# Optimization experiments

Hardware: AMD Instinct MI355X
Metric: run time of the kernel (lower is better)

Reference implementation:

```python
import jax, jax.numpy as jnp
import numpy as np

H = 4      # SSM / attn heads (d_model/headdim = 256/64)
WIN = 4    # attention window over bands


def _ln(x, g, b):
    m = jnp.mean(x, -1, keepdims=True)
    v = jnp.mean((x - m) ** 2, -1, keepdims=True)
    return (x - m) * jax.lax.rsqrt(v + 1e-5) * g + b


def setup_inputs() -> dict:
    key = jax.random.key(0)
    ks = jax.random.split(key, 24)
    def rn(i, shape, s=0.05):
        return jax.random.normal(ks[i], shape, jnp.float32) * s
    B, T, K, D = 2, 256, 8, 256
    return {
        "z": rn(0, (B, T, K, D), 1.0),
        "ln1_g": jnp.ones((D,), jnp.float32), "ln1_b": jnp.zeros((D,), jnp.float32),
        "Wx": rn(1, (D, D)), "conv_w": rn(2, (D, 4), 0.3), "Wz": rn(3, (D, D)),
        "Wb": rn(4, (D, H * 128)), "Wc": rn(5, (D, H * 128)), "Wdt": rn(6, (D, H)),
        "dt_bias": rn(7, (H,), 0.5), "A_log": rn(8, (H,), 0.5), "theta": rn(9, (H,), 1.0),
        "D_skip": rn(10, (H,), 1.0), "mimo_U": rn(11, (H, H), 0.5), "mimo_V": rn(12, (H, H), 0.5),
        "Wout": rn(13, (D, D)),
        "ln2_g": jnp.ones((D,), jnp.float32), "ln2_b": jnp.zeros((D,), jnp.float32),
        "attn_in_w": rn(14, (3 * D, D)), "attn_in_b": rn(15, (3 * D,), 0.02),
        "attn_out_w": rn(16, (D, D)), "attn_out_b": jnp.zeros((D,), jnp.float32),
        "ln3_g": jnp.ones((D,), jnp.float32), "ln3_b": jnp.zeros((D,), jnp.float32),
        "Wg": rn(17, (D, 4 * D)), "Wu": rn(18, (D, 4 * D)), "Wd": rn(19, (4 * D, D)),
    }


def _forward(z, ln1_g, ln1_b, Wx, conv_w, Wz, Wb, Wc, Wdt, dt_bias, A_log, theta,
             D_skip, mimo_U, mimo_V, Wout, ln2_g, ln2_b, attn_in_w, attn_in_b,
             attn_out_w, attn_out_b, ln3_g, ln3_b, Wg, Wu, Wd):
    B, T, K, D = z.shape
    P = D // H
    N = Wb.shape[1] // H
    # ---------- (a) intra-band Mamba3 (complex MIMO selective scan) ----------
    u = _ln(z, ln1_g, ln1_b)
    u = jnp.transpose(u, (0, 2, 1, 3)).reshape(B * K, T, D)   # [BK,T,D]
    x = u @ Wx
    # causal depthwise conv1d, kernel 4
    xp = jnp.pad(x, ((0, 0), (3, 0), (0, 0)))
    x = sum(xp[:, k:k + T, :] * conv_w[:, k] for k in range(4))
    x = jax.nn.silu(x)
    xh = x.reshape(B * K, T, H, P)
    Bm = (u @ Wb).reshape(B * K, T, H, N)
    Cm = (u @ Wc).reshape(B * K, T, H, N)
    Mmix = mimo_U @ mimo_V.T                                  # rank-r cross-head coupling
    Bm = jnp.einsum('hg,btgn->bthn', Mmix, Bm)
    dt = jax.nn.softplus(u @ Wdt + dt_bias)                   # [BK,T,H]
    A = -jnp.exp(A_log)                                       # stable real decay
    mag = jnp.exp(dt * A)
    ph = dt * theta                                           # harmonic rotation
    ar, ai = mag * jnp.cos(ph), mag * jnp.sin(ph)
    xs = tuple(jnp.moveaxis(t, 1, 0) for t in (xh, Bm, Cm, dt, ar, ai))
    h0 = jnp.zeros((B * K, H, N, P), x.dtype)

    def step(carry, s):
        h_re, h_im = carry
        xt, bt, ct, dtt, art, ait = s
        dBx = (dtt[:, :, None, None] * bt[:, :, :, None]) * xt[:, :, None, :]
        nr = art[:, :, None, None] * h_re - ait[:, :, None, None] * h_im + dBx
        ni = art[:, :, None, None] * h_im + ait[:, :, None, None] * h_re
        return (nr, ni), jnp.einsum('bhn,bhnp->bhp', ct, nr)   # Re(C . h)

    _, ys = jax.lax.scan(step, (h0, h0), xs)                  # ys: [T,BK,H,P]
    y = jnp.moveaxis(ys, 0, 1) + D_skip[None, None, :, None] * xh
    y = y.reshape(B * K, T, D) * jax.nn.silu(u @ Wz)
    y = y @ Wout
    z = z + jnp.transpose(y.reshape(B, K, T, D), (0, 2, 1, 3))
    # ---------- (b) inter-band windowed attention ----------
    zn = _ln(z, ln2_g, ln2_b).reshape(B * T, K, D)
    qkv = zn @ attn_in_w.T + attn_in_b
    q, k_, v = jnp.split(qkv, 3, axis=-1)
    hd = D // H
    def hs(t):
        return t.reshape(B * T, K // WIN, WIN, H, hd).transpose(0, 1, 3, 2, 4)
    q, k_, v = hs(q), hs(k_), hs(v)
    s = jnp.einsum('mwhqd,mwhkd->mwhqk', q, k_) * jnp.float32(1.0 / np.sqrt(hd))
    a = jax.nn.softmax(s, axis=-1)
    o = jnp.einsum('mwhqk,mwhkd->mwhqd', a, v).transpose(0, 1, 3, 2, 4).reshape(B * T, K, D)
    z = z + (o @ attn_out_w.T + attn_out_b).reshape(B, T, K, D)
    # ---------- (c) SwiGLU FFN ----------
    zf = _ln(z, ln3_g, ln3_b)
    z = z + (jax.nn.silu(zf @ Wg) * (zf @ Wu)) @ Wd
    return z


def reference(z, ln1_g, ln1_b, Wx, conv_w, Wz, Wb, Wc, Wdt, dt_bias, A_log, theta,
              D_skip, mimo_U, mimo_V, Wout, ln2_g, ln2_b, attn_in_w, attn_in_b,
              attn_out_w, attn_out_b, ln3_g, ln3_b, Wg, Wu, Wd):
    return _forward(z, ln1_g, ln1_b, Wx, conv_w, Wz, Wb, Wc, Wdt, dt_bias, A_log,
                    theta, D_skip, mimo_U, mimo_V, Wout, ln2_g, ln2_b, attn_in_w,
                    attn_in_b, attn_out_w, attn_out_b, ln3_g, ln3_b, Wg, Wu, Wd)
```

## Files before the change

### kernel.cpp

```cpp
#include <hip/hip_runtime.h>
#include <hip/hip_bf16.h>
#include <math.h>

typedef __hip_bfloat16 bf16;
typedef __attribute__((ext_vector_type(8))) short s16x8;
typedef __attribute__((ext_vector_type(4))) float f32x4;

__device__ __forceinline__ float siluf(float x) { return x / (1.f + __expf(-x)); }
__device__ __forceinline__ float bits2f(unsigned short u) {
    union { float f; unsigned i; } v; v.i = ((unsigned)u) << 16; return v.f;
}
__device__ __forceinline__ unsigned short f2bits(float f) {
    return (unsigned short)__bfloat16_as_ushort(__float2bfloat16(f));
}

#define KFL 1024
#define OFF_UB   (768*KFL)
#define OFF_DTV  (1280*KFL)
#define OFF_BMB  (1344*KFL)
#define OFF_CMB  (2368*KFL)
#define OFF_ZGB  (3392*KFL)
#define OFF_XB   (3904*KFL)
#define OFF_X2T  (4928*KFL)
#define OFF_P    (5440*KFL)
#define OFF_YGB  (7488*KFL)
#define OFF_Z2   (8000*KFL)
#define OFF_ZFB  (9024*KFL)
#define OFF_GG   OFF_BMB

#define W_BCZX 0
#define W_OUT  393216
#define W_QKV  458752
#define W_AO   655360
#define W_GU   720896
#define W_D    1245184

__global__ __launch_bounds__(256) void prep_ln1_kernel(
    const float* __restrict__ Wx, const float* __restrict__ Wb,
    const float* __restrict__ Wc, const float* __restrict__ Wz,
    const float* __restrict__ Wo, const float* __restrict__ Wqkv,
    const float* __restrict__ Wao, const float* __restrict__ Wg,
    const float* __restrict__ Wu, const float* __restrict__ Wd,
    const float* __restrict__ U, const float* __restrict__ V,
    unsigned short* __restrict__ wout,
    const float* __restrict__ z, const float* __restrict__ g1,
    const float* __restrict__ b1, const float* __restrict__ Wdt,
    const float* __restrict__ dt_bias,
    unsigned short* __restrict__ u, float4* __restrict__ dtv4)
{
    __shared__ __align__(16) float smem[64 * 65];
    int blk = blockIdx.x;
    int tid = threadIdx.x;
    if (blk < 368) {
        if (blk >= 304) {
            int off = blk - 304;
            const float* src; int dst, base;
            if (off < 48) { src = Wqkv; dst = W_QKV; base = off * 4096; }
            else          { src = Wao;  dst = W_AO;  base = (off - 48) * 4096; }
            #pragma unroll
            for (int i = 0; i < 16; i++) {
                int idx = base + tid + i * 256;
                wout[dst + idx] = f2bits(src[idx]);
            }
            return;
        }
        float* lds = smem;
        const float* src; int srcN, n0, sc0, k0, dstoff, dstK, mix = 0, t;
        if (blk < 32)       { t = blk;       src = Wb; srcN = 512;  dstoff = W_BCZX; dstK = 256;
                              n0 = (t >> 2) * 64;        sc0 = 0; k0 = (t & 3) * 64; mix = 1; }
        else if (blk < 64)  { t = blk - 32;  src = Wc; srcN = 512;  dstoff = W_BCZX; dstK = 256;
                              n0 = 512 + (t >> 2) * 64;  sc0 = (t >> 2) * 64; k0 = (t & 3) * 64; }
        else if (blk < 80)  { t = blk - 64;  src = Wz; srcN = 256;  dstoff = W_BCZX; dstK = 256;
                              n0 = 1024 + (t >> 2) * 64; sc0 = (t >> 2) * 64; k0 = (t & 3) * 64; }
        else if (blk < 96)  { t = blk - 80;  src = Wx; srcN = 256;  dstoff = W_BCZX; dstK = 256;
                              n0 = 1280 + (t >> 2) * 64; sc0 = (t >> 2) * 64; k0 = (t & 3) * 64; }
        else if (blk < 112) { t = blk - 96;  src = Wo; srcN = 256;  dstoff = W_OUT;  dstK = 256;
                              n0 = (t >> 2) * 64;        sc0 = n0; k0 = (t & 3) * 64; }
        else if (blk < 176) { t = blk - 112; src = Wg; srcN = 1024; dstoff = W_GU;   dstK = 256;
                              n0 = (t >> 2) * 64;        sc0 = n0; k0 = (t & 3) * 64; }
        else if (blk < 240) { t = blk - 176; src = Wu; srcN = 1024; dstoff = W_GU;   dstK = 256;
                              n0 = 1024 + (t >> 2) * 64; sc0 = (t >> 2) * 64; k0 = (t & 3) * 64; }
        else                { t = blk - 240; src = Wd; srcN = 256;  dstoff = W_D;    dstK = 1024;
                              n0 = (t >> 4) * 64;        sc0 = n0; k0 = (t & 15) * 64; }
        if (mix) {
            int h = n0 >> 7, scol = n0 & 127;
            float mm[4];
            #pragma unroll
            for (int g = 0; g < 4; g++) {
                float s = 0.f;
                #pragma unroll
                for (int j = 0; j < 4; j++) s += U[h * 4 + j] * V[g * 4 + j];
                mm[g] = s;
            }
            #pragma unroll
            for (int i = 0; i < 16; i++) {
                int idx = tid + i * 256;
                int kk = idx >> 6, nn = idx & 63;
                const float* row = src + (size_t)(k0 + kk) * 512 + scol + nn;
                lds[kk * 65 + nn] = mm[0] * row[0] + mm[1] * row[128]
                                  + mm[2] * row[256] + mm[3] * row[384];
            }
        } else {
            #pragma unroll
            for (int i = 0; i < 16; i++) {
                int idx = tid + i * 256;
                int kk = idx >> 6, nn = idx & 63;
                lds[kk * 65 + nn] = src[(size_t)(k0 + kk) * srcN + sc0 + nn];
            }
        }
        __syncthreads();
        #pragma unroll
        for (int i = 0; i < 16; i++) {
            int idx = tid + i * 256;
            int nn = idx >> 6, kk = idx & 63;
            wout[dstoff + (size_t)(n0 + nn) * dstK + k0 + kk] = f2bits(lds[kk * 65 + nn]);
        }
        return;
    }
    int r = blk - 368;
    float* lds = smem;
    float* dts = smem + 4;
    int t = r & 255, bk = r >> 8;
    int b_ = bk >> 3, k = bk & 7;
    int srcr = ((b_ * 256 + t) * 8 + k) * 256;
    int d = tid;
    float x = z[srcr + d];
    float v = x;
    #pragma unroll
    for (int off = 32; off; off >>= 1) v += __shfl_xor(v, off, 64);
    if ((d & 63) == 0) lds[d >> 6] = v;
    __syncthreads();
    float mean = (lds[0] + lds[1] + lds[2] + lds[3]) * (1.f / 256.f);
    __syncthreads();
    float c = x - mean;
    v = c * c;
    #pragma unroll
    for (int off = 32; off; off >>= 1) v += __shfl_xor(v, off, 64);
    if ((d & 63) == 0) lds[d >> 6] = v;
    __syncthreads();
    float var = (lds[0] + lds[1] + lds[2] + lds[3]) * (1.f / 256.f);
    float uval = c * rsqrtf(var + 1e-5f) * g1[d] + b1[d];
    u[r * 256 + d] = f2bits(uval);
    float4 wv = *(const float4*)(Wdt + d * 4);
    float q0 = uval * wv.x, q1 = uval * wv.y, q2 = uval * wv.z, q3 = uval * wv.w;
    #pragma unroll
    for (int off = 32; off; off >>= 1) {
        q0 += __shfl_xor(q0, off, 64);
        q1 += __shfl_xor(q1, off, 64);
        q2 += __shfl_xor(q2, off, 64);
        q3 += __shfl_xor(q3, off, 64);
    }
    if ((d & 63) == 0) {
        int w = d >> 6;
        dts[w * 4 + 0] = q0; dts[w * 4 + 1] = q1;
        dts[w * 4 + 2] = q2; dts[w * 4 + 3] = q3;
    }
    __syncthreads();
    if (d == 0) {
        float dv[4];
        #pragma unroll
        for (int h = 0; h < 4; h++) {
            float xx = dts[h] + dts[4 + h] + dts[8 + h] + dts[12 + h] + dt_bias[h];
            dv[h] = (xx > 20.f) ? xx : log1pf(__expf(xx));
        }
        dtv4[r] = make_float4(dv[0], dv[1], dv[2], dv[3]);
    }
}

__global__ __launch_bounds__(256) void gemm_bczx(
    const unsigned short* __restrict__ A, const unsigned short* __restrict__ Bt,
    unsigned short* __restrict__ bmb, unsigned short* __restrict__ cmb,
    unsigned short* __restrict__ zgb, unsigned short* __restrict__ xb)
{
    __shared__ __align__(16) unsigned short As[64 * 72];
    __shared__ __align__(16) unsigned short Bs[128 * 72];
    const int K = 256;
    int tid = threadIdx.x;
    int n0 = blockIdx.x * 128, m0 = blockIdx.y * 64;
    int w = tid >> 6, l = tid & 63;
    int mwave = (w >> 1) * 32, nwave = (w & 1) * 64;
    f32x4 acc[2][4] = {};
    int srow = tid >> 3, sc = (tid & 7) * 8;
    const unsigned short* Ap = A + (size_t)(m0 + srow) * K + sc;
    const unsigned short* Bp = Bt + (size_t)(n0 + srow) * K + sc;
    int lq = l & 15, lh = l >> 4;
    uint4 a0 = *(const uint4*)(Ap);
    uint4 a1 = *(const uint4*)(Ap + (size_t)32 * K);
    uint4 b0 = *(const uint4*)(Bp);
    uint4 b1 = *(const uint4*)(Bp + (size_t)32 * K);
    uint4 b2 = *(const uint4*)(Bp + (size_t)64 * K);
    uint4 b3 = *(const uint4*)(Bp + (size_t)96 * K);
    for (int k0 = 0; k0 < K; k0 += 64) {
        if (k0) __syncthreads();
        *(uint4*)&As[srow * 72 + sc] = a0;
        *(uint4*)&As[(srow + 32) * 72 + sc] = a1;
        *(uint4*)&Bs[srow * 72 + sc] = b0;
        *(uint4*)&Bs[(srow + 32) * 72 + sc] = b1;
        *(uint4*)&Bs[(srow + 64) * 72 + sc] = b2;
        *(uint4*)&Bs[(srow + 96) * 72 + sc] = b3;
        __syncthreads();
        if (k0 + 64 < K) {
            a0 = *(const uint4*)(Ap + k0 + 64);
            a1 = *(const uint4*)(Ap + (size_t)32 * K + k0 + 64);
            b0 = *(const uint4*)(Bp + k0 + 64);
            b1 = *(const uint4*)(Bp + (size_t)32 * K + k0 + 64);
            b2 = *(const uint4*)(Bp + (size_t)64 * K + k0 + 64);
            b3 = *(const uint4*)(Bp + (size_t)96 * K + k0 + 64);
        }
        #pragma unroll
        for (int kk = 0; kk < 2; kk++) {
            int kof = kk * 32 + lh * 8;
            s16x8 bfr[4];
            #pragma unroll
            for (int nf = 0; nf < 4; nf++)
                bfr[nf] = *(const s16x8*)&Bs[(nwave + nf * 16 + lq) * 72 + kof];
            #pragma unroll
            for (int mf = 0; mf < 2; mf++) {
                s16x8 af = *(const s16x8*)&As[(mwave + mf * 16 + lq) * 72 + kof];
                #pragma unroll
                for (int nf = 0; nf < 4; nf++)
                    acc[mf][nf] = __builtin_amdgcn_mfma_f32_16x16x32_bf16(af, bfr[nf], acc[mf][nf], 0, 0, 0);
            }
        }
    }
    #pragma unroll
    for (int mf = 0; mf < 2; mf++) {
        #pragma unroll
        for (int nf = 0; nf < 4; nf++) {
            int n = n0 + nwave + nf * 16 + lq;
            #pragma unroll
            for (int r = 0; r < 4; r++) {
                int m = m0 + mwave + mf * 16 + lh * 4 + r;
                float v = acc[mf][nf][r];
                if (n < 512)       bmb[(size_t)m * 512 + n] = f2bits(v);
                else if (n < 1024) cmb[(size_t)m * 512 + (n - 512)] = f2bits(v);
                else if (n < 1280) zgb[(size_t)m * 256 + (n - 1024)] = f2bits(siluf(v));
                else               xb[(size_t)m * 256 + (n - 1280)] = f2bits(v);
            }
        }
    }
}

__global__ __launch_bounds__(256) void s_conv_kernel(
    const unsigned short* __restrict__ cmb, const unsigned short* __restrict__ bmb,
    const float4* __restrict__ dtv4, const float* __restrict__ A_log,
    const float* __restrict__ theta, unsigned short* __restrict__ P,
    const unsigned short* __restrict__ xb, const float* __restrict__ cw,
    unsigned short* __restrict__ x2t)
{
    __shared__ __align__(16) char smem[39936];
    int blk = blockIdx.x;
    int tid = threadIdx.x;
    if (blk >= 192) {
        int c = blk - 192;
        int bhid = c >> 2, tt = c & 3;
        int bk = bhid >> 2, h = bhid & 3;
        int t0 = tt * 64;
        float* tile = (float*)smem;
        #pragma unroll
        for (int i = 0; i < 17; i++) {
            int idx = tid + i * 256;
            if (idx < 67 * 64) {
                int tr = idx >> 6, dd = idx & 63;
                int t = t0 - 3 + tr;
                tile[tr * 65 + dd] = (t >= 0)
                    ? bits2f(xb[(size_t)(bk * 256 + t) * 256 + h * 64 + dd]) : 0.f;
            }
        }
        __syncthreads();
        int wv_ = tid >> 6, lt = tid & 63;
        #pragma unroll 4
        for (int pi = 0; pi < 16; pi++) {
            int p = wv_ * 16 + pi;
            float4 wv = *(const float4*)(cw + (h * 64 + p) * 4);
            float acc = tile[lt * 65 + p] * wv.x + tile[(lt + 1) * 65 + p] * wv.y +
                        tile[(lt + 2) * 65 + p] * wv.z + tile[(lt + 3) * 65 + p] * wv.w;
            x2t[(size_t)(bhid * 64 + p) * 256 + t0 + lt] = f2bits(siluf(acc));
        }
        return;
    }
    int map = blk >> 6;
    int bh = blk & 63;
    int bx = (map == 2) ? 1 : 0;
    int by = (map == 0) ? 0 : 1;
    int bk = bh >> 2, h = bh & 3;
    unsigned short* As = (unsigned short*)smem;
    unsigned short* Bs = As + 128 * 72;
    float* mAs = (float*)(smem + 36864);
    float* phs = mAs + 256;
    float* dss = phs + 256;
    int srow = tid >> 3, sc = (tid & 7) * 8;
    const unsigned short* Ap = cmb + (size_t)(bk * 256 + by * 128 + srow) * 512 + h * 128 + sc;
    const unsigned short* Bp = bmb + (size_t)(bk * 256 + bx * 128 + srow) * 512 + h * 128 + sc;
    uint4 a0 = *(const uint4*)(Ap);
    uint4 a1 = *(const uint4*)(Ap + (size_t)32 * 512);
    uint4 a2 = *(const uint4*)(Ap + (size_t)64 * 512);
    uint4 a3 = *(const uint4*)(Ap + (size_t)96 * 512);
    uint4 b0 = *(const uint4*)(Bp);
    uint4 b1 = *(const uint4*)(Bp + (size_t)32 * 512);
    uint4 b2 = *(const uint4*)(Bp + (size_t)64 * 512);
    uint4 b3 = *(const uint4*)(Bp + (size_t)96 * 512);
    {
        float4 dv = dtv4[bk * 256 + tid];
        float dth = (h == 0) ? dv.x : (h == 1) ? dv.y : (h == 2) ? dv.z : dv.w;
        float Ah = -__expf(A_log[h]);
        float th = theta[h];
        float a = dth * Ah, p = dth * th;
        dss[tid] = dth;
        int lane = tid & 63, wv = tid >> 6;
        #pragma unroll
        for (int off = 1; off < 64; off <<= 1) {
            float ta = __shfl_up(a, off, 64);
            float tp = __shfl_up(p, off, 64);
            if (lane >= off) { a += ta; p += tp; }
        }
        if (lane == 63) { mAs[wv] = a; phs[wv] = p; }
        __syncthreads();
        float offA = 0.f, offP = 0.f;
        #pragma unroll
        for (int j = 0; j < 3; j++)
            if (j < wv) { offA += mAs[j]; offP += phs[j]; }
        __syncthreads();
        mAs[tid] = a + offA;
        phs[tid] = p + offP;
        __syncthreads();
    }
    int w = tid >> 6, l = tid & 63;
    int mwave = (w >> 1) * 64, nwave = (w & 1) * 64;
    int lq = l & 15, lh = l >> 4;
    unsigned short* Pout = P + (size_t)bh * 65536;
    f32x4 acc[4][4] = {};
    for (int k0 = 0; k0 < 128; k0 += 64) {
        __syncthreads();
        *(uint4*)&As[srow * 72 + sc] = a0;
        *(uint4*)&As[(srow + 32) * 72 + sc] = a1;
        *(uint4*)&As[(srow + 64) * 72 + sc] = a2;
        *(uint4*)&As[(srow + 96) * 72 + sc] = a3;
        *(uint4*)&Bs[srow * 72 + sc] = b0;
        *(uint4*)&Bs[(srow + 32) * 72 + sc] = b1;
        *(uint4*)&Bs[(srow + 64) * 72 + sc] = b2;
        *(uint4*)&Bs[(srow + 96) * 72 + sc] = b3;
        __syncthreads();
        if (k0 + 64 < 128) {
            a0 = *(const uint4*)(Ap + k0 + 64);
            a1 = *(const uint4*)(Ap + (size_t)32 * 512 + k0 + 64);
            a2 = *(const uint4*)(Ap + (size_t)64 * 512 + k0 + 64);
            a3 = *(const uint4*)(Ap + (size_t)96 * 512 + k0 + 64);
            b0 = *(const uint4*)(Bp + k0 + 64);
            b1 = *(const uint4*)(Bp + (size_t)32 * 512 + k0 + 64);
            b2 = *(const uint4*)(Bp + (size_t)64 * 512 + k0 + 64);
            b3 = *(const uint4*)(Bp + (size_t)96 * 512 + k0 + 64);
        }
        #pragma unroll
        for (int kk = 0; kk < 2; kk++) {
            int kof = kk * 32 + lh * 8;
            s16x8 bfr[4];
            #pragma unroll
            for (int nf = 0; nf < 4; nf++)
                bfr[nf] = *(const s16x8*)&Bs[(nwave + nf * 16 + lq) * 72 + kof];
            #pragma unroll
            for (int mf = 0; mf < 4; mf++) {
                s16x8 af = *(const s16x8*)&As[(mwave + mf * 16 + lq) * 72 + kof];
                #pragma unroll
                for (int nf = 0; nf < 4; nf++)
                    acc[mf][nf] = __builtin_amdgcn_mfma_f32_16x16x32_bf16(af, bfr[nf], acc[mf][nf], 0, 0, 0);
            }
        }
    }
    #pragma unroll
    for (int mf = 0; mf < 4; mf++) {
        float tmv[4], tpv[4]; int tg[4];
        #pragma unroll
        for (int r = 0; r < 4; r++) {
            tg[r] = by * 128 + mwave + mf * 16 + lh * 4 + r;
            tmv[r] = mAs[tg[r]];
            tpv[r] = phs[tg[r]];
        }
        #pragma unroll
        for (int nf = 0; nf < 4; nf++) {
            int s = bx * 128 + nwave + nf * 16 + lq;
            float ms = mAs[s];
            float ps = phs[s];
            float ds = dss[s];
            #pragma unroll
            for (int r = 0; r < 4; r++) {
                float wgt = (s <= tg[r])
                    ? __expf(tmv[r] - ms) * __cosf(tpv[r] - ps) * ds : 0.f;
                Pout[tg[r] * 256 + s] = f2bits(acc[mf][nf][r] * wgt);
            }
        }
    }
}

__global__ __launch_bounds__(256) void gemm_y(
    const unsigned short* __restrict__ P, const unsigned short* __restrict__ x2t,
    const unsigned short* __restrict__ zgb, const float* __restrict__ Dsk,
    unsigned short* __restrict__ ygb)
{
    int by = blockIdx.x, bh = blockIdx.y;
    int bk = bh >> 2, h = bh & 3;
    int t0 = by * 32;
    int tid = threadIdx.x;
    int w = tid >> 6, l = tid & 63;
    int mw = (w >> 1) * 16, nw = (w & 1) * 32;
    int lq = l & 15, lh = l >> 4;
    __shared__ __align__(16) unsigned short As[32 * 72];
    __shared__ __align__(16) unsigned short Bs[64 * 72];
    f32x4 acc[2] = {};
    int srow = tid >> 3, sc = (tid & 7) * 8;
    const unsigned short* Ap = P + (size_t)bh * 65536 + (size_t)(t0 + srow) * 256 + sc;
    const unsigned short* Bp = x2t + (size_t)bh * 16384 + (size_t)srow * 256 + sc;
    int kmax = ((by >> 1) + 1) * 64;
    uint4 a0 = *(const uint4*)(Ap);
    uint4 b0 = *(const uint4*)(Bp);
    uint4 b1 = *(const uint4*)(Bp + (size_t)32 * 256);
    for (int k0 = 0; k0 < kmax; k0 += 64) {
        if (k0) __syncthreads();
        *(uint4*)&As[(srow & 31) * 72 + sc] = a0;
        *(uint4*)&Bs[srow * 72 + sc] = b0;
        *(uint4*)&Bs[(srow + 32) * 72 + sc] = b1;
        __syncthreads();
        if (k0 + 64 < kmax) {
            a0 = *(const uint4*)(Ap + k0 + 64);
            b0 = *(const uint4*)(Bp + k0 + 64);
            b1 = *(const uint4*)(Bp + (size_t)32 * 256 + k0 + 64);
        }
        #pragma unroll
        for (int kk = 0; kk < 2; kk++) {
            int kof = kk * 32 + lh * 8;
            s16x8 af = *(const s16x8*)&As[(mw + lq) * 72 + kof];
            #pragma unroll
            for (int nf = 0; nf < 2; nf++) {
                s16x8 bf = *(const s16x8*)&Bs[(nw + nf * 16 + lq) * 72 + kof];
                acc[nf] = __builtin_amdgcn_mfma_f32_16x16x32_bf16(af, bf, acc[nf], 0, 0, 0);
            }
        }
    }
    float dsk = Dsk[h];
    #pragma unroll
    for (int nf = 0; nf < 2; nf++) {
        int p = nw + nf * 16 + lq;
        #pragma unroll
        for (int r = 0; r < 4; r++) {
            int t = t0 + mw + lh * 4 + r;
            float xv = bits2f(x2t[(size_t)bh * 16384 + p * 256 + t]);
            float zg = bits2f(zgb[(size_t)(bk * 256 + t) * 256 + h * 64 + p]);
            ygb[(size_t)(bk * 256 + t) * 256 + h * 64 + p] =
                f2bits((acc[nf][r] + dsk * xv) * zg);
        }
    }
}

__global__ __launch_bounds__(512) void mid_kernel(
    const unsigned short* __restrict__ ygb, const unsigned short* __restrict__ wts,
    const float* __restrict__ zin,
    const float* __restrict__ g2, const float* __restrict__ b2,
    const float* __restrict__ qbias, const float* __restrict__ obias,
    const float* __restrict__ g3, const float* __restrict__ b3,
    float* __restrict__ z2, unsigned short* __restrict__ zfb)
{
    __shared__ __align__(16) char smem[65024];
    unsigned short* Bs = (unsigned short*)smem;
    unsigned short* As = (unsigned short*)(smem + 36864);
    unsigned short* zn = (unsigned short*)(smem + 39168);
    float* z1s = (float*)(smem + 47616);
    float (*partS)[8] = (float(*)[8])(smem + 64000);
    float (*partQ)[8] = (float(*)[8])(smem + 64512);
    unsigned short* qk = (unsigned short*)smem;

    const int K = 256;
    int tid = threadIdx.x;
    int m0 = blockIdx.x * 16;
    int w = tid >> 6, l = tid & 63;
    int nw = w * 32;
    int lq = l & 15, lh = l >> 4;
    int srow = tid >> 3, sc = (tid & 7) * 8;

    const unsigned short* BpO  = wts + W_OUT + (size_t)srow * K + sc;
    const unsigned short* BpQ0 = wts + W_QKV + (size_t)srow * K + sc;
    const unsigned short* BpQ1 = BpQ0 + (size_t)256 * K;
    const unsigned short* BpQ2 = BpQ0 + (size_t)512 * K;
    const unsigned short* BpA  = wts + W_AO + (size_t)srow * K + sc;

    uint4 wA0, wA1, wA2, wA3, wB0, wB1, wB2, wB3;

#define LOADW(P, BASE, KO) do { \
    P##0 = *(const uint4*)((BASE) + (KO)); \
    P##1 = *(const uint4*)((BASE) + (size_t)64 * K + (KO)); \
    P##2 = *(const uint4*)((BASE) + (size_t)128 * K + (KO)); \
    P##3 = *(const uint4*)((BASE) + (size_t)192 * K + (KO)); \
} while (0)
#define STORE_BS(P) do { \
    *(uint4*)&Bs[srow * 72 + sc] = P##0; \
    *(uint4*)&Bs[(srow + 64) * 72 + sc] = P##1; \
    *(uint4*)&Bs[(srow + 128) * 72 + sc] = P##2; \
    *(uint4*)&Bs[(srow + 192) * 72 + sc] = P##3; \
} while (0)
#define MM_ZN(AQ, KO) do { \
    _Pragma("unroll") \
    for (int kk = 0; kk < 2; kk++) { \
        int kof = kk * 32 + lh * 8; \
        s16x8 af = *(const s16x8*)&zn[lq * 264 + (KO) + kof]; \
        _Pragma("unroll") \
        for (int nf = 0; nf < 2; nf++) { \
            s16x8 bf = *(const s16x8*)&Bs[(nw + nf * 16 + lq) * 72 + kof]; \
            AQ[nf] = __builtin_amdgcn_mfma_f32_16x16x32_bf16(af, bf, AQ[nf], 0, 0, 0); \
        } \
    } \
} while (0)
#define MM_AS(AQ) do { \
    _Pragma("unroll") \
    for (int kk = 0; kk < 2; kk++) { \
        int kof = kk * 32 + lh * 8; \
        s16x8 af = *(const s16x8*)&As[lq * 72 + kof]; \
        _Pragma("unroll") \
        for (int nf = 0; nf < 2; nf++) { \
            s16x8 bf = *(const s16x8*)&Bs[(nw + nf * 16 + lq) * 72 + kof]; \
            AQ[nf] = __builtin_amdgcn_mfma_f32_16x16x32_bf16(af, bf, AQ[nf], 0, 0, 0); \
        } \
    } \
} while (0)

    f32x4 acc1[2] = {};
    {
        int rb = m0 + (srow & 15);
        int irow = ((rb >> 11) * 8 + (rb & 7)) * 256 + ((rb >> 3) & 255);
        const unsigned short* Ap = ygb + (size_t)irow * K + sc;
        LOADW(wA, BpO, 0);
        LOADW(wB, BpO, 64);
        uint4 aP = *(const uint4*)(Ap);
        uint4 aQ;
        __syncthreads();
        if (tid < 128) *(uint4*)&As[srow * 72 + sc] = aP;
        STORE_BS(wA);
        __syncthreads();
        aQ = *(const uint4*)(Ap + 64);
        LOADW(wA, BpO, 128);
        MM_AS(acc1);
        __syncthreads();
        if (tid < 128) *(uint4*)&As[srow * 72 + sc] = aQ;
        STORE_BS(wB);
        __syncthreads();
        aP = *(const uint4*)(Ap + 128);
        LOADW(wB, BpO, 192);
        MM_AS(acc1);
        __syncthreads();
        if (tid < 128) *(uint4*)&As[srow * 72 + sc] = aP;
        STORE_BS(wA);
        __syncthreads();
        aQ = *(const uint4*)(Ap + 192);
        LOADW(wA, BpQ0, 0);
        MM_AS(acc1);
        __syncthreads();
        if (tid < 128) *(uint4*)&As[srow * 72 + sc] = aQ;
        STORE_BS(wB);
        __syncthreads();
        LOADW(wB, BpQ0, 64);
        MM_AS(acc1);
        #pragma unroll
        for (int r = 0; r < 4; r++) {
            int row = lh * 4 + r;
            float s = 0.f, q = 0.f;
            #pragma unroll
            for (int nf = 0; nf < 2; nf++) {
                float v = acc1[nf][r] + zin[(size_t)(m0 + row) * 256 + nw + nf * 16 + lq];
                acc1[nf][r] = v;
                s += v; q += v * v;
            }
            #pragma unroll
            for (int off = 1; off < 16; off <<= 1) {
                s += __shfl_xor(s, off, 64);
                q += __shfl_xor(q, off, 64);
            }
            if (lq == 0) { partS[row][w] = s; partQ[row][w] = q; }
        }
        __syncthreads();
        float gv[2], bbv[2];
        #pragma unroll
        for (int nf = 0; nf < 2; nf++) {
            gv[nf] = g2[nw + nf * 16 + lq];
            bbv[nf] = b2[nw + nf * 16 + lq];
        }
        #pragma unroll
        for (int r = 0; r < 4; r++) {
            int row = lh * 4 + r;
            float sum = 0.f, sq = 0.f;
            #pragma unroll
            for (int j = 0; j < 8; j++) { sum += partS[row][j]; sq += partQ[row][j]; }
            float mean = sum * (1.f / 256.f);
            float var = sq * (1.f / 256.f) - mean * mean;
            float rstd = rsqrtf(var + 1e-5f);
            #pragma unroll
            for (int nf = 0; nf < 2; nf++) {
                int n = nw + nf * 16 + lq;
                float v = acc1[nf][r];
                z1s[row * 256 + n] = v;
                zn[row * 264 + n] = f2bits((v - mean) * rstd * gv[nf] + bbv[nf]);
            }
        }
    }

    f32x4 aq0[2] = {}, aq1[2] = {}, aq2[2] = {};
#define RND(P, AQ, KO, NBASE, NKO) do { \
    __syncthreads(); \
    STORE_BS(P); \
    __syncthreads(); \
    LOADW(P, NBASE, NKO); \
    MM_ZN(AQ, KO); \
} while (0)
#define RND_NL(P, AQ, KO) do { \
    __syncthreads(); \
    STORE_BS(P); \
    __syncthreads(); \
    MM_ZN(AQ, KO); \
} while (0)
    RND(wA, aq0, 0,   BpQ0, 128);
    RND(wB, aq0, 64,  BpQ0, 192);
    RND(wA, aq0, 128, BpQ1, 0);
    RND(wB, aq0, 192, BpQ1, 64);
    RND(wA, aq1, 0,   BpQ1, 128);
    RND(wB, aq1, 64,  BpQ1, 192);
    RND(wA, aq1, 128, BpQ2, 0);
    RND(wB, aq1, 192, BpQ2, 64);
    RND(wA, aq2, 0,   BpQ2, 128);
    RND(wB, aq2, 64,  BpQ2, 192);
    RND(wA, aq2, 128, BpA, 0);
    RND(wB, aq2, 192, BpA, 64);

    __syncthreads();
#define QKV_STORE(PIDX, AQ) do { \
    _Pragma("unroll") \
    for (int nf = 0; nf < 2; nf++) { \
        int n = (PIDX) * 256 + nw + nf * 16 + lq; \
        float bb = qbias[n]; \
        _Pragma("unroll") \
        for (int r = 0; r < 4; r++) \
            qk[(lh * 4 + r) * 776 + n] = f2bits(AQ[nf][r] + bb); \
    } \
} while (0)
    QKV_STORE(0, aq0);
    QKV_STORE(1, aq1);
    QKV_STORE(2, aq2);
#undef QKV_STORE
    __syncthreads();
    {
        int hh = w & 3;
        int half = w >> 2;
        int d = l;
        #pragma unroll
        for (int wi = 0; wi < 2; wi++) {
            int w4 = half * 2 + wi;
            int r0 = w4 * 4;
            float qv[4], kv[4], vv[4];
            #pragma unroll
            for (int j = 0; j < 4; j++) {
                qv[j] = bits2f(qk[(r0 + j) * 776 + hh * 64 + d]);
                kv[j] = bits2f(qk[(r0 + j) * 776 + 256 + hh * 64 + d]);
                vv[j] = bits2f(qk[(r0 + j) * 776 + 512 + hh * 64 + d]);
            }
            float sc_[4][4];
            #pragma unroll
            for (int qi = 0; qi < 4; qi++)
                #pragma unroll
                for (int ki = 0; ki < 4; ki++) {
                    float v = qv[qi] * kv[ki];
                    #pragma unroll
                    for (int off = 32; off; off >>= 1) v += __shfl_xor(v, off, 64);
                    sc_[qi][ki] = v * 0.125f;
                }
            #pragma unroll
            for (int qi = 0; qi < 4; qi++) {
                float mx = fmaxf(fmaxf(sc_[qi][0], sc_[qi][1]), fmaxf(sc_[qi][2], sc_[qi][3]));
                float e0 = __expf(sc_[qi][0] - mx), e1 = __expf(sc_[qi][1] - mx);
                float e2 = __expf(sc_[qi][2] - mx), e3 = __expf(sc_[qi][3] - mx);
                float inv = 1.f / (e0 + e1 + e2 + e3);
                float ov = (e0 * vv[0] + e1 * vv[1] + e2 * vv[2] + e3 * vv[3]) * inv;
                zn[(r0 + qi) * 264 + hh * 64 + d] = f2bits(ov);
            }
        }
    }

    {
        f32x4 ac4[2] = {};
        RND(wA, ac4, 0,  BpA, 128);
        RND(wB, ac4, 64, BpA, 192);
        RND_NL(wA, ac4, 128);
        RND_NL(wB, ac4, 192);
        float bv[2], gv[2], bbv[2];
        #pragma unroll
        for (int nf = 0; nf < 2; nf++) {
            int n = nw + nf * 16 + lq;
            bv[nf] = obias[n];
            gv[nf] = g3[n];
            bbv[nf] = b3[n];
        }
        #pragma unroll
        for (int r = 0; r < 4; r++) {
            int row = lh * 4 + r;
            float s = 0.f, q = 0.f;
            #pragma unroll
            for (int nf = 0; nf < 2; nf++) {
                float v = ac4[nf][r] + bv[nf] + z1s[row * 256 + nw + nf * 16 + lq];
                ac4[nf][r] = v;
                s += v; q += v * v;
            }
            #pragma unroll
            for (int off = 1; off < 16; off <<= 1) {
                s += __shfl_xor(s, off, 64);
                q += __shfl_xor(q, off, 64);
            }
            if (lq == 0) { partS[row][w] = s; partQ[row][w] = q; }
        }
        __syncthreads();
        #pragma unroll
        for (int r = 0; r < 4; r++) {
            int row = lh * 4 + r;
            float sum = 0.f, sq = 0.f;
            #pragma unroll
            for (int j = 0; j < 8; j++) { sum += partS[row][j]; sq += partQ[row][j]; }
            float mean = sum * (1.f / 256.f);
            float var = sq * (1.f / 256.f) - mean * mean;
            float rstd = rsqrtf(var + 1e-5f);
            size_t ro = (size_t)(m0 + row) * 256;
            #pragma unroll
            for (int nf = 0; nf < 2; nf++) {
                int n = nw + nf * 16 + lq;
                float v = ac4[nf][r];
                z2[ro + n] = v;
                zfb[ro + n] = f2bits((v - mean) * rstd * gv[nf] + bbv[nf]);
            }
        }
    }
#undef RND
#undef RND_NL
#undef LOADW
#undef STORE_BS
#undef MM_ZN
#undef MM_AS
}

__global__ __launch_bounds__(256) void gemm_gu2(
    const unsigned short* __restrict__ A, const unsigned short* __restrict__ Wgu,
    unsigned short* __restrict__ gg)
{
    const int K = 256;
    __shared__ __align__(16) unsigned short As[64 * 72];
    __shared__ __align__(16) unsigned short Bgs[64 * 72];
    __shared__ __align__(16) unsigned short Bus[64 * 72];
    int tid = threadIdx.x;
    int n0 = blockIdx.x * 64, m0 = blockIdx.y * 64;
    int w = tid >> 6, l = tid & 63;
    int mwave = (w >> 1) * 32, nwave = (w & 1) * 32;
    int lq = l & 15, lh = l >> 4;
    f32x4 ag[2][2] = {}, au[2][2] = {};
    int srow = tid >> 3, sc = (tid & 7) * 8;
    const unsigned short* Ap = A + (size_t)(m0 + srow) * K + sc;
    const unsigned short* Bgp = Wgu + (size_t)(n0 + srow) * K + sc;
    const unsigned short* Bup = Wgu + (size_t)(1024 + n0 + srow) * K + sc;
    uint4 a0 = *(const uint4*)(Ap);
    uint4 a1 = *(const uint4*)(Ap + (size_t)32 * K);
    uint4 bg0 = *(const uint4*)(Bgp);
    uint4 bg1 = *(const uint4*)(Bgp + (size_t)32 * K);
    uint4 bu0 = *(const uint4*)(Bup);
    uint4 bu1 = *(const uint4*)(Bup + (size_t)32 * K);
    for (int k0 = 0; k0 < K; k0 += 64) {
        if (k0) __syncthreads();
        *(uint4*)&As[srow * 72 + sc] = a0;
        *(uint4*)&As[(srow + 32) * 72 + sc] = a1;
        *(uint4*)&Bgs[srow * 72 + sc] = bg0;
        *(uint4*)&Bgs[(srow + 32) * 72 + sc] = bg1;
        *(uint4*)&Bus[srow * 72 + sc] = bu0;
        *(uint4*)&Bus[(srow + 32) * 72 + sc] = bu1;
        __syncthreads();
        if (k0 + 64 < K) {
            a0 = *(const uint4*)(Ap + k0 + 64);
            a1 = *(const uint4*)(Ap + (size_t)32 * K + k0 + 64);
            bg0 = *(const uint4*)(Bgp + k0 + 64);
            bg1 = *(const uint4*)(Bgp + (size_t)32 * K + k0 + 64);
            bu0 = *(const uint4*)(Bup + k0 + 64);
            bu1 = *(const uint4*)(Bup + (size_t)32 * K + k0 + 64);
        }
        #pragma unroll
        for (int kk = 0; kk < 2; kk++) {
            int kof = kk * 32 + lh * 8;
            s16x8 bgr[2], bur[2];
            #pragma unroll
            for (int nf = 0; nf < 2; nf++) {
                bgr[nf] = *(const s16x8*)&Bgs[(nwave + nf * 16 + lq) * 72 + kof];
                bur[nf] = *(const s16x8*)&Bus[(nwave + nf * 16 + lq) * 72 + kof];
            }
            #pragma unroll
            for (int mf = 0; mf < 2; mf++) {
                s16x8 af = *(const s16x8*)&As[(mwave + mf * 16 + lq) * 72 + kof];
                #pragma unroll
                for (int nf = 0; nf < 2; nf++) {
                    ag[mf][nf] = __builtin_amdgcn_mfma_f32_16x16x32_bf16(af, bgr[nf], ag[mf][nf], 0, 0, 0);
                    au[mf][nf] = __builtin_amdgcn_mfma_f32_16x16x32_bf16(af, bur[nf], au[mf][nf], 0, 0, 0);
                }
            }
        }
    }
    #pragma unroll
    for (int mf = 0; mf < 2; mf++) {
        #pragma unroll
        for (int nf = 0; nf < 2; nf++) {
            int n = n0 + nwave + nf * 16 + lq;
            #pragma unroll
            for (int r = 0; r < 4; r++) {
                int m = m0 + mwave + mf * 16 + lh * 4 + r;
                gg[(size_t)m * 1024 + n] = f2bits(siluf(ag[mf][nf][r]) * au[mf][nf][r]);
            }
        }
    }
}

__global__ __launch_bounds__(256) void gemm_d2(
    const unsigned short* __restrict__ gg, const unsigned short* __restrict__ Bt,
    const float* __restrict__ resid, float* __restrict__ out)
{
    __shared__ __align__(16) unsigned short As[64 * 72];
    __shared__ __align__(16) unsigned short Bs[32 * 72];
    const int K = 1024, N = 256;
    int tid = threadIdx.x;
    int n0 = blockIdx.x * 32, m0 = blockIdx.y * 64;
    int w = tid >> 6, l = tid & 63;
    int mw = (w >> 1) * 32, nw = (w & 1) * 16;
    f32x4 acc[2] = {};
    int srow = tid >> 3, sc = (tid & 7) * 8;
    const unsigned short* Ap = gg + (size_t)(m0 + srow) * K + sc;
    const unsigned short* Bp = Bt + (size_t)(n0 + (srow & 31)) * K + sc;
    int lq = l & 15, lh = l >> 4;
    uint4 xA0 = *(const uint4*)(Ap);
    uint4 xA1 = *(const uint4*)(Ap + (size_t)32 * K);
    uint4 yA  = *(const uint4*)(Bp);
    uint4 xB0 = *(const uint4*)(Ap + 64);
    uint4 xB1 = *(const uint4*)(Ap + (size_t)32 * K + 64);
    uint4 yB  = *(const uint4*)(Bp + 64);
    for (int k0 = 0; k0 < K; k0 += 128) {
        __syncthreads();
        *(uint4*)&As[srow * 72 + sc] = xA0;
        *(uint4*)&As[(srow + 32) * 72 + sc] = xA1;
        *(uint4*)&Bs[(srow & 31) * 72 + sc] = yA;
        __syncthreads();
        if (k0 + 128 < K) {
            xA0 = *(const uint4*)(Ap + k0 + 128);
            xA1 = *(const uint4*)(Ap + (size_t)32 * K + k0 + 128);
            yA  = *(const uint4*)(Bp + k0 + 128);
        }
        #pragma unroll
        for (int kk = 0; kk < 2; kk++) {
            int kof = kk * 32 + lh * 8;
            s16x8 bf = *(const s16x8*)&Bs[(nw + lq) * 72 + kof];
            #pragma unroll
            for (int mf = 0; mf < 2; mf++) {
                s16x8 af = *(const s16x8*)&As[(mw + mf * 16 + lq) * 72 + kof];
                acc[mf] = __builtin_amdgcn_mfma_f32_16x16x32_bf16(af, bf, acc[mf], 0, 0, 0);
            }
        }
        __syncthreads();
        *(uint4*)&As[srow * 72 + sc] = xB0;
        *(uint4*)&As[(srow + 32) * 72 + sc] = xB1;
        *(uint4*)&Bs[(srow & 31) * 72 + sc] = yB;
        __syncthreads();
        if (k0 + 192 < K) {
            xB0 = *(const uint4*)(Ap + k0 + 192);
            xB1 = *(const uint4*)(Ap + (size_t)32 * K + k0 + 192);
            yB  = *(const uint4*)(Bp + k0 + 192);
        }
        #pragma unroll
        for (int kk = 0; kk < 2; kk++) {
            int kof = kk * 32 + lh * 8;
            s16x8 bf = *(const s16x8*)&Bs[(nw + lq) * 72 + kof];
            #pragma unroll
            for (int mf = 0; mf < 2; mf++) {
                s16x8 af = *(const s16x8*)&As[(mw + mf * 16 + lq) * 72 + kof];
                acc[mf] = __builtin_amdgcn_mfma_f32_16x16x32_bf16(af, bf, acc[mf], 0, 0, 0);
            }
        }
    }
    int n = n0 + nw + lq;
    #pragma unroll
    for (int mf = 0; mf < 2; mf++) {
        #pragma unroll
        for (int r = 0; r < 4; r++) {
            int m = m0 + mw + mf * 16 + lh * 4 + r;
            out[(size_t)m * N + n] = acc[mf][r] + resid[(size_t)m * N + n];
        }
    }
}

extern "C" void kernel_launch(void* const* d_in, const int* in_sizes, int n_in,
                              void* d_out, int out_size, void* d_ws, size_t ws_size,
                              hipStream_t stream)
{
    const float* z         = (const float*)d_in[0];
    const float* ln1_g     = (const float*)d_in[1];
    const float* ln1_b     = (const float*)d_in[2];
    const float* Wx        = (const float*)d_in[3];
    const float* conv_w    = (const float*)d_in[4];
    const float* Wz        = (const float*)d_in[5];
    const float* Wb        = (const float*)d_in[6];
    const float* Wc        = (const float*)d_in[7];
    const float* Wdt       = (const float*)d_in[8];
    const float* dt_bias   = (const float*)d_in[9];
    const float* A_log     = (const float*)d_in[10];
    const float* theta     = (const float*)d_in[11];
    const float* D_skip    = (const float*)d_in[12];
    const float* mimo_U    = (const float*)d_in[13];
    const float* mimo_V    = (const float*)d_in[14];
    const float* Wout      = (const float*)d_in[15];
    const float* ln2_g     = (const float*)d_in[16];
    const float* ln2_b     = (const float*)d_in[17];
    const float* attn_in_w = (const float*)d_in[18];
    const float* attn_in_b = (const float*)d_in[19];
    const float* attn_out_w= (const float*)d_in[20];
    const float* attn_out_b= (const float*)d_in[21];
    const float* ln3_g     = (const float*)d_in[22];
    const float* ln3_b     = (const float*)d_in[23];
    const float* Wg        = (const float*)d_in[24];
    const float* Wu        = (const float*)d_in[25];
    const float* Wd        = (const float*)d_in[26];

    float* W = (float*)d_ws;
    unsigned short* wts = (unsigned short*)W;
    unsigned short* ub  = (unsigned short*)(W + OFF_UB);
    float4* dtv4        = (float4*)(W + OFF_DTV);
    unsigned short* bmb = (unsigned short*)(W + OFF_BMB);
    unsigned short* cmb = (unsigned short*)(W + OFF_CMB);
    unsigned short* zgb = (unsigned short*)(W + OFF_ZGB);
    unsigned short* xb  = (unsigned short*)(W + OFF_XB);
    unsigned short* x2t = (unsigned short*)(W + OFF_X2T);
    unsigned short* pbuf= (unsigned short*)(W + OFF_P);
    unsigned short* ygb = (unsigned short*)(W + OFF_YGB);
    float* z2           = W + OFF_Z2;
    unsigned short* zfb = (unsigned short*)(W + OFF_ZFB);
    unsigned short* gg  = (unsigned short*)(W + OFF_GG);

    prep_ln1_kernel<<<4464, 256, 0, stream>>>(
        Wx, Wb, Wc, Wz, Wout, attn_in_w, attn_out_w, Wg, Wu, Wd, mimo_U, mimo_V,
        wts, z, ln1_g, ln1_b, Wdt, dt_bias, ub, dtv4);
    gemm_bczx<<<dim3(12, 64), 256, 0, stream>>>(ub, wts + W_BCZX, bmb, cmb, zgb, xb);
    s_conv_kernel<<<448, 256, 0, stream>>>(cmb, bmb, dtv4, A_log, theta, pbuf,
                                           xb, conv_w, x2t);
    gemm_y<<<dim3(8, 64), 256, 0, stream>>>(pbuf, x2t, zgb, D_skip, ygb);
    mid_kernel<<<256, 512, 0, stream>>>(ygb, wts, z, ln2_g, ln2_b,
                                        attn_in_b, attn_out_b, ln3_g, ln3_b,
                                        z2, zfb);
    gemm_gu2<<<dim3(16, 64), 256, 0, stream>>>(zfb, wts + W_GU, gg);
    gemm_d2<<<dim3(8, 64), 256, 0, stream>>>(gg, wts + W_D, z2, (float*)d_out);
}
```

Measured before the change: 190.5 us.

## Fuse SSM score, conv and Y GEMM into one kernel keeping P in LDS

Merges the score/conv kernel and the gemm_y kernel into a single score_kernel. Each block computes a 64-row band of the causal decay-weighted C·B^T matrix into shared memory, recomputes the depthwise conv plus SiLU of x per chunk, then multiplies P by the conv output and applies the D-skip and gate. This removes the global P and x2t round trips and one kernel launch. The cost is redundant conv recomputation across blocks, only 256 blocks, and uneven causal work per block.

```diff
diff --git a/kernel.cpp b/kernel.cpp
--- a/kernel.cpp
+++ b/kernel.cpp
@@ -21,8 +21,6 @@
 #define OFF_CMB  (2368*KFL)
 #define OFF_ZGB  (3392*KFL)
 #define OFF_XB   (3904*KFL)
-#define OFF_X2T  (4928*KFL)
-#define OFF_P    (5440*KFL)
 #define OFF_YGB  (7488*KFL)
 #define OFF_Z2   (8000*KFL)
 #define OFF_ZFB  (9024*KFL)
@@ -241,144 +239,107 @@
     }
 }
 
-__global__ __launch_bounds__(256) void s_conv_kernel(
+__global__ __launch_bounds__(512) void score_kernel(
     const unsigned short* __restrict__ cmb, const unsigned short* __restrict__ bmb,
     const float4* __restrict__ dtv4, const float* __restrict__ A_log,
-    const float* __restrict__ theta, unsigned short* __restrict__ P,
+    const float* __restrict__ theta,
     const unsigned short* __restrict__ xb, const float* __restrict__ cw,
-    unsigned short* __restrict__ x2t)
+    const unsigned short* __restrict__ zgb, const float* __restrict__ Dsk,
+    unsigned short* __restrict__ ygb)
 {
-    __shared__ __align__(16) char smem[39936];
-    int blk = blockIdx.x;
-    int tid = threadIdx.x;
-    if (blk >= 192) {
-        int c = blk - 192;
-        int bhid = c >> 2, tt = c & 3;
-        int bk = bhid >> 2, h = bhid & 3;
-        int t0 = tt * 64;
-        float* tile = (float*)smem;
-        #pragma unroll
-        for (int i = 0; i < 17; i++) {
-            int idx = tid + i * 256;
-            if (idx < 67 * 64) {
-                int tr = idx >> 6, dd = idx & 63;
-                int t = t0 - 3 + tr;
-                tile[tr * 65 + dd] = (t >= 0)
-                    ? bits2f(xb[(size_t)(bk * 256 + t) * 256 + h * 64 + dd]) : 0.f;
-            }
-        }
-        __syncthreads();
-        int wv_ = tid >> 6, lt = tid & 63;
-        #pragma unroll 4
-        for (int pi = 0; pi < 16; pi++) {
-            int p = wv_ * 16 + pi;
-            float4 wv = *(const float4*)(cw + (h * 64 + p) * 4);
-            float acc = tile[lt * 65 + p] * wv.x + tile[(lt + 1) * 65 + p] * wv.y +
-                        tile[(lt + 2) * 65 + p] * wv.z + tile[(lt + 3) * 65 + p] * wv.w;
-            x2t[(size_t)(bhid * 64 + p) * 256 + t0 + lt] = f2bits(siluf(acc));
-        }
-        return;
-    }
-    int map = blk >> 6;
-    int bh = blk & 63;
-    int bx = (map == 2) ? 1 : 0;
-    int by = (map == 0) ? 0 : 1;
-    int bk = bh >> 2, h = bh & 3;
-    unsigned short* As = (unsigned short*)smem;
-    unsigned short* Bs = As + 128 * 72;
-    float* mAs = (float*)(smem + 36864);
+    __shared__ __align__(16) char smem[62976];
+    unsigned short* Pl  = (unsigned short*)smem;
+    unsigned short* As2 = (unsigned short*)(smem + 33792);
+    unsigned short* Bs  = (unsigned short*)(smem + 50688);
+    unsigned short* Xc  = (unsigned short*)(smem + 33792);
+    float* mAs = (float*)(smem + 59904);
     float* phs = mAs + 256;
     float* dss = phs + 256;
-    int srow = tid >> 3, sc = (tid & 7) * 8;
-    const unsigned short* Ap = cmb + (size_t)(bk * 256 + by * 128 + srow) * 512 + h * 128 + sc;
-    const unsigned short* Bp = bmb + (size_t)(bk * 256 + bx * 128 + srow) * 512 + h * 128 + sc;
-    uint4 a0 = *(const uint4*)(Ap);
-    uint4 a1 = *(const uint4*)(Ap + (size_t)32 * 512);
-    uint4 a2 = *(const uint4*)(Ap + (size_t)64 * 512);
-    uint4 a3 = *(const uint4*)(Ap + (size_t)96 * 512);
-    uint4 b0 = *(const uint4*)(Bp);
-    uint4 b1 = *(const uint4*)(Bp + (size_t)32 * 512);
-    uint4 b2 = *(const uint4*)(Bp + (size_t)64 * 512);
-    uint4 b3 = *(const uint4*)(Bp + (size_t)96 * 512);
+
+    int by = blockIdx.x;
+    int bh = blockIdx.y;
+    int bk = bh >> 2, h = bh & 3;
+    int tid = threadIdx.x;
+    int w = tid >> 6, l = tid & 63;
+    int lq = l & 15, lh = l >> 4;
+    int srow2 = tid >> 3, sc2 = (tid & 7) * 8;
+
+    uint4 ax0, ax1;
     {
-        float4 dv = dtv4[bk * 256 + tid];
-        float dth = (h == 0) ? dv.x : (h == 1) ? dv.y : (h == 2) ? dv.z : dv.w;
+        int uid0 = tid, uid1 = tid + 512;
+        ax0 = *(const uint4*)(cmb + (size_t)(bk * 256 + by * 64 + (uid0 >> 4)) * 512 + h * 128 + (uid0 & 15) * 8);
+        ax1 = *(const uint4*)(cmb + (size_t)(bk * 256 + by * 64 + (uid1 >> 4)) * 512 + h * 128 + (uid1 & 15) * 8);
+    }
+    uint4 bl = *(const uint4*)(bmb + (size_t)(bk * 256 + srow2) * 512 + h * 128 + sc2);
+    float4 cwv = *(const float4*)(cw + (h * 64 + l) * 4);
+
+    {
+        float dth = 0.f;
+        if (tid < 256) {
+            float4 dv = dtv4[bk * 256 + tid];
+            dth = (h == 0) ? dv.x : (h == 1) ? dv.y : (h == 2) ? dv.z : dv.w;
+            dss[tid] = dth;
+        }
         float Ah = -__expf(A_log[h]);
         float th = theta[h];
-        float a = dth * Ah, p = dth * th;
-        dss[tid] = dth;
+        float sa = dth * Ah, sp = dth * th;
         int lane = tid & 63, wv = tid >> 6;
         #pragma unroll
         for (int off = 1; off < 64; off <<= 1) {
-            float ta = __shfl_up(a, off, 64);
-            float tp = __shfl_up(p, off, 64);
-            if (lane >= off) { a += ta; p += tp; }
-        }
-        if (lane == 63) { mAs[wv] = a; phs[wv] = p; }
+            float ta = __shfl_up(sa, off, 64);
+            float tp = __shfl_up(sp, off, 64);
+            if (lane >= off) { sa += ta; sp += tp; }
+        }
+        if (tid < 256 && lane == 63) { mAs[wv] = sa; phs[wv] = sp; }
         __syncthreads();
         float offA = 0.f, offP = 0.f;
         #pragma unroll
         for (int j = 0; j < 3; j++)
             if (j < wv) { offA += mAs[j]; offP += phs[j]; }
         __syncthreads();
-        mAs[tid] = a + offA;
-        phs[tid] = p + offP;
-        __syncthreads();
-    }
-    int w = tid >> 6, l = tid & 63;
-    int mwave = (w >> 1) * 64, nwave = (w & 1) * 64;
-    int lq = l & 15, lh = l >> 4;
-    unsigned short* Pout = P + (size_t)bh * 65536;
-    f32x4 acc[4][4] = {};
-    for (int k0 = 0; k0 < 128; k0 += 64) {
-        __syncthreads();
-        *(uint4*)&As[srow * 72 + sc] = a0;
-        *(uint4*)&As[(srow + 32) * 72 + sc] = a1;
-        *(uint4*)&As[(srow + 64) * 72 + sc] = a2;
-        *(uint4*)&As[(srow + 96) * 72 + sc] = a3;
-        *(uint4*)&Bs[srow * 72 + sc] = b0;
-        *(uint4*)&Bs[(srow + 32) * 72 + sc] = b1;
-        *(uint4*)&Bs[(srow + 64) * 72 + sc] = b2;
-        *(uint4*)&Bs[(srow + 96) * 72 + sc] = b3;
-        __syncthreads();
-        if (k0 + 64 < 128) {
-            a0 = *(const uint4*)(Ap + k0 + 64);
-            a1 = *(const uint4*)(Ap + (size_t)32 * 512 + k0 + 64);
-            a2 = *(const uint4*)(Ap + (size_t)64 * 512 + k0 + 64);
-            a3 = *(const uint4*)(Ap + (size_t)96 * 512 + k0 + 64);
-            b0 = *(const uint4*)(Bp + k0 + 64);
-            b1 = *(const uint4*)(Bp + (size_t)32 * 512 + k0 + 64);
-            b2 = *(const uint4*)(Bp + (size_t)64 * 512 + k0 + 64);
-            b3 = *(const uint4*)(Bp + (size_t)96 * 512 + k0 + 64);
-        }
-        #pragma unroll
-        for (int kk = 0; kk < 2; kk++) {
-            int kof = kk * 32 + lh * 8;
-            s16x8 bfr[4];
-            #pragma unroll
-            for (int nf = 0; nf < 4; nf++)
-                bfr[nf] = *(const s16x8*)&Bs[(nwave + nf * 16 + lq) * 72 + kof];
-            #pragma unroll
-            for (int mf = 0; mf < 4; mf++) {
-                s16x8 af = *(const s16x8*)&As[(mwave + mf * 16 + lq) * 72 + kof];
+        if (tid < 256) { mAs[tid] = sa + offA; phs[tid] = sp + offP; }
+    }
+    {
+        int uid0 = tid, uid1 = tid + 512;
+        *(uint4*)&As2[(uid0 >> 4) * 132 + (uid0 & 15) * 8] = ax0;
+        *(uint4*)&As2[(uid1 >> 4) * 132 + (uid1 & 15) * 8] = ax1;
+    }
+
+    int mwP = (w & 3) * 16, nwP = (w >> 2) * 32;
+    for (int nc = 0; nc <= by; nc++) {
+        f32x4 pacc[2] = {};
+        #pragma unroll
+        for (int k0 = 0; k0 < 128; k0 += 64) {
+            __syncthreads();
+            *(uint4*)&Bs[srow2 * 72 + sc2] = bl;
+            __syncthreads();
+            {
+                int nnc = nc, nk0 = k0 + 64;
+                if (nk0 == 128) { nnc = nc + 1; nk0 = 0; }
+                if (nnc <= by)
+                    bl = *(const uint4*)(bmb + (size_t)(bk * 256 + nnc * 64 + srow2) * 512 + h * 128 + nk0 + sc2);
+            }
+            #pragma unroll
+            for (int kk = 0; kk < 2; kk++) {
+                int kof = kk * 32 + lh * 8;
+                s16x8 af = *(const s16x8*)&As2[(mwP + lq) * 132 + k0 + kof];
                 #pragma unroll
-                for (int nf = 0; nf < 4; nf++)
-                    acc[mf][nf] = __builtin_amdgcn_mfma_f32_16x16x32_bf16(af, bfr[nf], acc[mf][nf], 0, 0, 0);
-            }
-        }
-    }
-    #pragma unroll
-    for (int mf = 0; mf < 4; mf++) {
+                for (int nf = 0; nf < 2; nf++) {
+                    s16x8 bf = *(const s16x8*)&Bs[(nwP + nf * 16 + lq) * 72 + kof];
+                    pacc[nf] = __builtin_amdgcn_mfma_f32_16x16x32_bf16(af, bf, pacc[nf], 0, 0, 0);
+                }
+            }
+        }
         float tmv[4], tpv[4]; int tg[4];
         #pragma unroll
         for (int r = 0; r < 4; r++) {
-            tg[r] = by * 128 + mwave + mf * 16 + lh * 4 + r;
+            tg[r] = by * 64 + mwP + lh * 4 + r;
             tmv[r] = mAs[tg[r]];
             tpv[r] = phs[tg[r]];
         }
         #pragma unroll
-        for (int nf = 0; nf < 4; nf++) {
-            int s = bx * 128 + nwave + nf * 16 + lq;
+        for (int nf = 0; nf < 2; nf++) {
+            int s = nc * 64 + nwP + nf * 16 + lq;
             float ms = mAs[s];
             float ps = phs[s];
             float ds = dss[s];
@@ -386,67 +347,59 @@
             for (int r = 0; r < 4; r++) {
                 float wgt = (s <= tg[r])
                     ? __expf(tmv[r] - ms) * __cosf(tpv[r] - ps) * ds : 0.f;
-                Pout[tg[r] * 256 + s] = f2bits(acc[mf][nf][r] * wgt);
-            }
-        }
-    }
-}
-
-__global__ __launch_bounds__(256) void gemm_y(
-    const unsigned short* __restrict__ P, const unsigned short* __restrict__ x2t,
-    const unsigned short* __restrict__ zgb, const float* __restrict__ Dsk,
-    unsigned short* __restrict__ ygb)
-{
-    int by = blockIdx.x, bh = blockIdx.y;
-    int bk = bh >> 2, h = bh & 3;
-    int t0 = by * 32;
-    int tid = threadIdx.x;
-    int w = tid >> 6, l = tid & 63;
-    int mw = (w >> 1) * 16, nw = (w & 1) * 32;
-    int lq = l & 15, lh = l >> 4;
-    __shared__ __align__(16) unsigned short As[32 * 72];
-    __shared__ __align__(16) unsigned short Bs[64 * 72];
-    f32x4 acc[2] = {};
-    int srow = tid >> 3, sc = (tid & 7) * 8;
-    const unsigned short* Ap = P + (size_t)bh * 65536 + (size_t)(t0 + srow) * 256 + sc;
-    const unsigned short* Bp = x2t + (size_t)bh * 16384 + (size_t)srow * 256 + sc;
-    int kmax = ((by >> 1) + 1) * 64;
-    uint4 a0 = *(const uint4*)(Ap);
-    uint4 b0 = *(const uint4*)(Bp);
-    uint4 b1 = *(const uint4*)(Bp + (size_t)32 * 256);
-    for (int k0 = 0; k0 < kmax; k0 += 64) {
-        if (k0) __syncthreads();
-        *(uint4*)&As[(srow & 31) * 72 + sc] = a0;
-        *(uint4*)&Bs[srow * 72 + sc] = b0;
-        *(uint4*)&Bs[(srow + 32) * 72 + sc] = b1;
-        __syncthreads();
-        if (k0 + 64 < kmax) {
-            a0 = *(const uint4*)(Ap + k0 + 64);
-            b0 = *(const uint4*)(Bp + k0 + 64);
-            b1 = *(const uint4*)(Bp + (size_t)32 * 256 + k0 + 64);
-        }
-        #pragma unroll
-        for (int kk = 0; kk < 2; kk++) {
-            int kof = kk * 32 + lh * 8;
-            s16x8 af = *(const s16x8*)&As[(mw + lq) * 72 + kof];
-            #pragma unroll
-            for (int nf = 0; nf < 2; nf++) {
-                s16x8 bf = *(const s16x8*)&Bs[(nw + nf * 16 + lq) * 72 + kof];
-                acc[nf] = __builtin_amdgcn_mfma_f32_16x16x32_bf16(af, bf, acc[nf], 0, 0, 0);
+                Pl[(mwP + lh * 4 + r) * 264 + s] = f2bits(pacc[nf][r] * wgt);
+            }
+        }
+    }
+
+    int mwY = (w >> 2) * 32, nwY = (w & 3) * 16;
+    f32x4 yacc[2] = {};
+    float xvv[2][4];
+    for (int sc = 0; sc <= by; sc++) {
+        __syncthreads();
+        #pragma unroll
+        for (int i = 0; i < 8; i++) {
+            int tl = w + i * 8;
+            int t_abs = sc * 64 + tl;
+            float a = 0.f;
+            #pragma unroll
+            for (int j = 0; j < 4; j++) {
+                int tr = t_abs - 3 + j;
+                float xj = (tr >= 0) ? bits2f(xb[(size_t)(bk * 256 + tr) * 256 + h * 64 + l]) : 0.f;
+                float wj = (j == 0) ? cwv.x : (j == 1) ? cwv.y : (j == 2) ? cwv.z : cwv.w;
+                a += xj * wj;
+            }
+            Xc[l * 72 + tl] = f2bits(siluf(a));
+        }
+        __syncthreads();
+        if (sc == by) {
+            #pragma unroll
+            for (int mf = 0; mf < 2; mf++)
+                #pragma unroll
+                for (int r = 0; r < 4; r++)
+                    xvv[mf][r] = bits2f(Xc[(nwY + lq) * 72 + mwY + mf * 16 + lh * 4 + r]);
+        }
+        #pragma unroll
+        for (int ks = 0; ks < 2; ks++) {
+            int kof = ks * 32 + lh * 8;
+            s16x8 bf = *(const s16x8*)&Xc[(nwY + lq) * 72 + kof];
+            #pragma unroll
+            for (int mf = 0; mf < 2; mf++) {
+                s16x8 af = *(const s16x8*)&Pl[(mwY + mf * 16 + lq) * 264 + sc * 64 + kof];
+                yacc[mf] = __builtin_amdgcn_mfma_f32_16x16x32_bf16(af, bf, yacc[mf], 0, 0, 0);
             }
         }
     }
     float dsk = Dsk[h];
     #pragma unroll
-    for (int nf = 0; nf < 2; nf++) {
-        int p = nw + nf * 16 + lq;
+    for (int mf = 0; mf < 2; mf++) {
         #pragma unroll
         for (int r = 0; r < 4; r++) {
-            int t = t0 + mw + lh * 4 + r;
-            float xv = bits2f(x2t[(size_t)bh * 16384 + p * 256 + t]);
-            float zg = bits2f(zgb[(size_t)(bk * 256 + t) * 256 + h * 64 + p]);
-            ygb[(size_t)(bk * 256 + t) * 256 + h * 64 + p] =
-                f2bits((acc[nf][r] + dsk * xv) * zg);
+            int t_abs = by * 64 + mwY + mf * 16 + lh * 4 + r;
+            int p = nwY + lq;
+            size_t off = (size_t)(bk * 256 + t_abs) * 256 + h * 64 + p;
+            float zg = bits2f(zgb[off]);
+            ygb[off] = f2bits((yacc[mf][r] + dsk * xvv[mf][r]) * zg);
         }
     }
 }
@@ -929,8 +882,6 @@
     unsigned short* cmb = (unsigned short*)(W + OFF_CMB);
     unsigned short* zgb = (unsigned short*)(W + OFF_ZGB);
     unsigned short* xb  = (unsigned short*)(W + OFF_XB);
-    unsigned short* x2t = (unsigned short*)(W + OFF_X2T);
-    unsigned short* pbuf= (unsigned short*)(W + OFF_P);
     unsigned short* ygb = (unsigned short*)(W + OFF_YGB);
     float* z2           = W + OFF_Z2;
     unsigned short* zfb = (unsigned short*)(W + OFF_ZFB);
@@ -940,9 +891,8 @@
         Wx, Wb, Wc, Wz, Wout, attn_in_w, attn_out_w, Wg, Wu, Wd, mimo_U, mimo_V,
         wts, z, ln1_g, ln1_b, Wdt, dt_bias, ub, dtv4);
     gemm_bczx<<<dim3(12, 64), 256, 0, stream>>>(ub, wts + W_BCZX, bmb, cmb, zgb, xb);
-    s_conv_kernel<<<448, 256, 0, stream>>>(cmb, bmb, dtv4, A_log, theta, pbuf,
-                                           xb, conv_w, x2t);
-    gemm_y<<<dim3(8, 64), 256, 0, stream>>>(pbuf, x2t, zgb, D_skip, ygb);
+    score_kernel<<<dim3(4, 64), 512, 0, stream>>>(cmb, bmb, dtv4, A_log, theta,
+                                                  xb, conv_w, zgb, D_skip, ygb);
     mid_kernel<<<256, 512, 0, stream>>>(ygb, wts, z, ln2_g, ln2_b,
                                         attn_in_b, attn_out_b, ln3_g, ln3_b,
                                         z2, zfb);
```

Result: slower. 212.8 us (+11.7%).
